# Kernel optimization log

Measured on AMD Instinct MI355X. Metric: run time of the kernel, lower is better.

## Reference

```python
import jax, jax.numpy as jnp
import numpy as np

# Upper-triangular index pattern used by convert_Avec_to_A (row-major triu of 4x4 -> 10 entries)
_TRIU_R, _TRIU_C = np.triu_indices(4)


def _A_vec_to_A(A_vec):
    """(B,10) -> (B,4,4) symmetric matrix, filling upper triangle row-major then mirroring."""
    B = A_vec.shape[0]
    A = jnp.zeros((B, 4, 4), dtype=A_vec.dtype)
    A = A.at[:, _TRIU_R, _TRIU_C].set(A_vec)
    A = A.at[:, _TRIU_C, _TRIU_R].set(A_vec)
    return A


def setup_inputs() -> dict:
    key = jax.random.key(0)
    k1, k2 = jax.random.split(key)
    B = 1048576
    A_vec_pred = jax.random.normal(k1, (B, 10), dtype=jnp.float32)
    q_target = jax.random.normal(k2, (B, 4), dtype=jnp.float32)
    q_target = q_target / jnp.linalg.norm(q_target, axis=-1, keepdims=True)  # unit quaternions
    return {"A_vec_pred": A_vec_pred, "q_target": q_target}


def reference(A_vec_pred, q_target):
    # A_vec_to_quat(-A_vec_pred): eigenvector of minimum eigenvalue of sym(-A_vec)
    A = _A_vec_to_A(-A_vec_pred)                 # (B,4,4)
    _, evs = jnp.linalg.eigh(A)                  # eigenvalues ascending; columns = eigenvectors
    q_pred = evs[:, :, 0]                        # (B,4) min-eigenvalue eigenvector (unit norm)
    # quat_chordal_squared_loss: d = min(||q-qt||, ||q+qt||); losses = 2*d^2*(4-d^2)
    d2 = jnp.minimum(jnp.sum((q_pred - q_target) ** 2, axis=-1),
                     jnp.sum((q_pred + q_target) ** 2, axis=-1))
    losses = 2.0 * d2 * (4.0 - d2)
    return losses.mean()
```

## Files before the change

### kernel.cpp

```cpp
#include <hip/hip_runtime.h>


#define TPB 256
#define PAIRS 2

typedef float vf4 __attribute__((ext_vector_type(4)));
typedef float vf2 __attribute__((ext_vector_type(2)));

struct Pair { vf4 f0, f1, f2, f3, f4, q0, q1; };

__device__ __forceinline__ void issue_loads(const float* a, const float* q,
                                            Pair& d) {
    unsigned long long aa = (unsigned long long)a;
    unsigned long long qq = (unsigned long long)q;
    asm volatile("global_load_dwordx4 %0, %1, off"           : "=v"(d.f0) : "v"(aa));
    asm volatile("global_load_dwordx4 %0, %1, off offset:16" : "=v"(d.f1) : "v"(aa));
    asm volatile("global_load_dwordx4 %0, %1, off offset:32" : "=v"(d.f2) : "v"(aa));
    asm volatile("global_load_dwordx4 %0, %1, off offset:48" : "=v"(d.f3) : "v"(aa));
    asm volatile("global_load_dwordx4 %0, %1, off offset:64" : "=v"(d.f4) : "v"(aa));
    asm volatile("global_load_dwordx4 %0, %1, off"           : "=v"(d.q0) : "v"(qq));
    asm volatile("global_load_dwordx4 %0, %1, off offset:16" : "=v"(d.q1) : "v"(qq));
}

__device__ __forceinline__ vf2 vmin2(vf2 a, vf2 b){ return __builtin_elementwise_min(a,b); }
__device__ __forceinline__ vf2 vmax2(vf2 a, vf2 b){ return __builtin_elementwise_max(a,b); }
__device__ __forceinline__ vf2 vabs2(vf2 a){ return __builtin_elementwise_abs(a); }
__device__ __forceinline__ vf2 splat2(float s){ vf2 r; r.x = s; r.y = s; return r; }
__device__ __forceinline__ vf2 rcp2(vf2 a){
    vf2 r; r.x = __builtin_amdgcn_rcpf(a.x); r.y = __builtin_amdgcn_rcpf(a.y);
    return r;
}

__device__ __forceinline__ vf2 solve_pair(const vf2 a[10],
                                          vf2 qx, vf2 qy, vf2 qz, vf2 qw) {
    vf2 m00 = -a[0], m01 = -a[1], m02 = -a[2], m03 = -a[3];
    vf2 m11 = -a[4], m12 = -a[5], m13 = -a[6];
    vf2 m22 = -a[7], m23 = -a[8], m33 = -a[9];

    vf2 e1 = m00 + m11 + m22 + m33;
    vf2 e2 = m00*m11 - m01*m01 + m00*m22 - m02*m02 + m00*m33 - m03*m03
           + m11*m22 - m12*m12 + m11*m33 - m13*m13 + m22*m33 - m23*m23;

    vf2 x01 = m02*m13 - m12*m03;
    vf2 x02 = m02*m23 - m22*m03;
    vf2 x03 = m02*m33 - m23*m03;
    vf2 x12 = m12*m23 - m22*m13;
    vf2 x13 = m12*m33 - m23*m13;
    vf2 x23 = m22*m33 - m23*m23;
    vf2 cw0 =  (m11*x23 - m12*x13 + m13*x12);
    vf2 cw1 = -(m01*x23 - m12*x03 + m13*x02);
    vf2 cw2 =  (m01*x13 - m11*x03 + m13*x01);
    vf2 cw3 = -(m01*x12 - m11*x02 + m12*x01);
    vf2 e4 = m00*cw0 + m01*cw1 + m02*cw2 + m03*cw3;

    vf2 e3 = cw0
           + (m00*x23 - m02*x03 + m03*x02)
           + (m00*(m11*m33 - m13*m13) - m01*(m01*m33 - m03*m13)
              + m03*(m01*m13 - m03*m11))
           + (m00*(m11*m22 - m12*m12) - m01*(m01*m22 - m02*m12)
              + m02*(m01*m12 - m02*m11));

    vf2 s0v = vabs2(m01) + vabs2(m02) + vabs2(m03);
    vf2 s1v = vabs2(m01) + vabs2(m12) + vabs2(m13);
    vf2 s2v = vabs2(m02) + vabs2(m12) + vabs2(m23);
    vf2 s3v = vabs2(m03) + vabs2(m13) + vabs2(m23);
    vf2 lo = vmin2(vmin2(m00 - s0v, m11 - s1v), vmin2(m22 - s2v, m33 - s3v))
           - splat2(1e-3f);
    vf2 hi = vmin2(vmin2(m00, m11), vmin2(m22, m33));
    vf2 lam = lo;
    vf2 ndpcap = splat2(-1e-12f);
    #pragma unroll
    for (int it = 0; it < 8; ++it) {
        vf2 p  = (((lam - e1)*lam + e2)*lam - e3)*lam + e4;
        vf2 dp = ((4.f*lam - 3.f*e1)*lam + 2.f*e2)*lam - e3;
        dp = vmin2(dp, ndpcap);
        lam = lam - p * rcp2(dp);
        lam = vmin2(vmax2(lam, lo), hi);
    }

    vf2 r00 = m00 - lam, r11 = m11 - lam, r22 = m22 - lam, r33 = m33 - lam;
    vf2 sm01 = m02*m13 - m12*m03;
    vf2 sm02 = m02*m23 - r22*m03;
    vf2 sm03 = m02*r33 - m23*m03;
    vf2 sm12 = m12*m23 - r22*m13;
    vf2 sm13 = m12*r33 - m23*m13;
    vf2 sm23 = r22*r33 - m23*m23;
    vf2 tm01 = r00*r11 - m01*m01;
    vf2 tm02 = r00*m12 - m02*m01;
    vf2 tm03 = r00*m13 - m03*m01;
    vf2 tm12 = m01*m12 - m02*r11;
    vf2 tm13 = m01*m13 - m03*r11;
    vf2 tm23 = m02*m13 - m03*m12;
    vf2 u0 = m01 - r00, u1 = r11 - m01, u2 = m12 - m02, u3 = m13 - m03;
    vf2 y0 = m03 - m02, y1 = m13 - m12, y2 = m23 - r22, y3 = r33 - m23;
    vf2 w0 =  (u1*sm23 - u2*sm13 + u3*sm12)
            + (y1*tm23 - y2*tm13 + y3*tm12);
    vf2 w1 = -(u0*sm23 - u2*sm03 + u3*sm02)
            - (y0*tm23 - y2*tm03 + y3*tm02);
    vf2 w2 =  (u0*sm13 - u1*sm03 + u3*sm01)
            + (y0*tm13 - y1*tm03 + y3*tm01);
    vf2 w3 = -(u0*sm12 - u1*sm02 + u2*sm01)
            - (y0*tm12 - y1*tm02 + y2*tm01);
    vf2 bn = w0*w0 + w1*w1 + w2*w2 + w3*w3;

    vf2 d = w0*qx + w1*qy + w2*qz + w3*qw;
    vf2 inv = rcp2(vmax2(bn, splat2(1e-20f)));
    vf2 loss = 8.f * (bn - d*d) * inv;
    return vmin2(vmax2(loss, splat2(0.f)), splat2(8.f));
}

__device__ __forceinline__ float det3s(float p, float q, float r,
                                       float s, float t, float u) {
    return p*(s*u - t*t) - q*(q*u - r*t) + r*(q*t - r*s);
}
__device__ __forceinline__ float solve_elem(const float a[10], float4 qt) {
    vf2 aa[10];
    #pragma unroll
    for (int i = 0; i < 10; ++i) { aa[i].x = a[i]; aa[i].y = a[i]; }
    vf2 L = solve_pair(aa, splat2(qt.x), splat2(qt.y), splat2(qt.z), splat2(qt.w));
    return L.x;
}

template <int CTRL, int ROW_MASK>
__device__ __forceinline__ float dpp_add(float v) {
    int t = __builtin_amdgcn_update_dpp(0, __builtin_bit_cast(int, v),
                                        CTRL, ROW_MASK, 0xf, true);
    return v + __builtin_bit_cast(float, t);
}

__device__ __forceinline__ float wave_sum(float v) {
    v = dpp_add<0x111, 0xf>(v);
    v = dpp_add<0x112, 0xf>(v);
    v = dpp_add<0x114, 0xf>(v);
    v = dpp_add<0x118, 0xf>(v);
    v = dpp_add<0x142, 0xa>(v);
    v = dpp_add<0x143, 0xc>(v);
    return __builtin_bit_cast(float,
        __builtin_amdgcn_readlane(__builtin_bit_cast(int, v), 63));
}

__global__ __launch_bounds__(TPB) void qcqp_loss_kernel(
    const float* __restrict__ A_vec, const float* __restrict__ q_t,
    float* __restrict__ part, int B, int T)
{
    int t = blockIdx.x * blockDim.x + threadIdx.x;
    int Ptot = B >> 1;
    float lsum = 0.f;

    Pair Pd, Nd;
    int curp = t;
    {
        int c = (curp < Ptot) ? curp : 0;
        issue_loads(A_vec + (size_t)c * 20, q_t + (size_t)c * 8, Pd);
    }
    int nxtp = curp;

    #define STEP(K, VMSTR)                                                    \
    {                                                                         \
        if ((K) + 1 < PAIRS) {                                                \
            nxtp = t + ((K) + 1) * T;                                         \
            int nc = (nxtp < Ptot) ? nxtp : 0;                                \
            issue_loads(A_vec + (size_t)nc * 20, q_t + (size_t)nc * 8, Nd);   \
        }                                                                     \
        asm volatile("s_waitcnt vmcnt(" VMSTR ")" ::: "memory");              \
        __builtin_amdgcn_sched_barrier(0);                                    \
        {                                                                     \
            bool ok = (curp < Ptot);                                          \
            vf2 aa[10];                                                       \
            aa[0] = (vf2){Pd.f0.x, Pd.f2.z};                                  \
            aa[1] = (vf2){Pd.f0.y, Pd.f2.w};                                  \
            aa[2] = (vf2){Pd.f0.z, Pd.f3.x};                                  \
            aa[3] = (vf2){Pd.f0.w, Pd.f3.y};                                  \
            aa[4] = (vf2){Pd.f1.x, Pd.f3.z};                                  \
            aa[5] = (vf2){Pd.f1.y, Pd.f3.w};                                  \
            aa[6] = (vf2){Pd.f1.z, Pd.f4.x};                                  \
            aa[7] = (vf2){Pd.f1.w, Pd.f4.y};                                  \
            aa[8] = (vf2){Pd.f2.x, Pd.f4.z};                                  \
            aa[9] = (vf2){Pd.f2.y, Pd.f4.w};                                  \
            vf2 qx = (vf2){Pd.q0.x, Pd.q1.x};                                 \
            vf2 qy = (vf2){Pd.q0.y, Pd.q1.y};                                 \
            vf2 qz = (vf2){Pd.q0.z, Pd.q1.z};                                 \
            vf2 qw = (vf2){Pd.q0.w, Pd.q1.w};                                 \
            vf2 L = solve_pair(aa, qx, qy, qz, qw);                           \
            lsum += ok ? (L.x + L.y) : 0.f;                                   \
        }                                                                     \
        Pd = Nd; curp = nxtp;                                                 \
    }

    STEP(0, "7")
    STEP(1, "0")
    #undef STEP

    float wsum = wave_sum(lsum);

    __shared__ float sm[TPB / 64];
    int lane = threadIdx.x & 63, wid = threadIdx.x >> 6;
    if (lane == 0) sm[wid] = wsum;
    __syncthreads();
    if (threadIdx.x == 0)
        part[blockIdx.x] = sm[0] + sm[1] + sm[2] + sm[3];
}

__global__ __launch_bounds__(TPB) void qcqp_reduce_kernel(
    const float* __restrict__ part, const float* __restrict__ A_vec,
    const float* __restrict__ q_t, float* __restrict__ out,
    int nparts, int B)
{
    float s = 0.f;
    for (int i = threadIdx.x; i < nparts; i += TPB)
        s += part[i];
    float wsum = wave_sum(s);

    __shared__ float sm[TPB / 64];
    int lane = threadIdx.x & 63, wid = threadIdx.x >> 6;
    if (lane == 0) sm[wid] = wsum;
    __syncthreads();
    if (threadIdx.x == 0) {
        float total = sm[0] + sm[1] + sm[2] + sm[3];
        if (B & 1) {
            const float* av = A_vec + (size_t)(B - 1) * 10;
            float2 v01 = *(const float2*)(av + 0);
            float2 v23 = *(const float2*)(av + 2);
            float2 v45 = *(const float2*)(av + 4);
            float2 v67 = *(const float2*)(av + 6);
            float2 v89 = *(const float2*)(av + 8);
            float a0[10] = {v01.x, v01.y, v23.x, v23.y, v45.x,
                            v45.y, v67.x, v67.y, v89.x, v89.y};
            float4 qt0 = *(const float4*)(q_t + (size_t)(B - 1) * 4);
            total += solve_elem(a0, qt0);
        }
        out[0] = total / (float)B;
    }
}

extern "C" void kernel_launch(void* const* d_in, const int* in_sizes, int n_in,
                              void* d_out, int out_size, void* d_ws, size_t ws_size,
                              hipStream_t stream)
{
    const float* A_vec = (const float*)d_in[0];
    const float* q_t   = (const float*)d_in[1];
    int B = in_sizes[0] / 10;
    float* part = (float*)d_ws;

    int Ptot = B >> 1;
    int nblocks = (Ptot + TPB * PAIRS - 1) / (TPB * PAIRS);
    int T = nblocks * TPB;
    qcqp_loss_kernel<<<nblocks, TPB, 0, stream>>>(A_vec, q_t, part, B, T);
    qcqp_reduce_kernel<<<1, TPB, 0, stream>>>(part, A_vec, q_t,
                                              (float*)d_out, nblocks, B);
}
```

Baseline: 18.55 us.

## Cut Newton iterations to six and fuse final reduction via atomics

Lowers the Newton iteration count for the minimum-eigenvalue root from 8 to 6, which trims ALU work per pair. It also removes the separate reduce kernel: each block atomically adds its scaled partial sum into the output, which is zeroed by a memset beforehand. The odd tail element now runs in thread 0 of the main kernel. Fewer iterations risk a less accurate eigenvalue for poorly conditioned matrices, and the atomics make the float summation order nondeterministic.

```diff
diff --git a/kernel.cpp b/kernel.cpp
--- a/kernel.cpp
+++ b/kernel.cpp
@@ -70,7 +70,7 @@
     vf2 lam = lo;
     vf2 ndpcap = splat2(-1e-12f);
     #pragma unroll
-    for (int it = 0; it < 8; ++it) {
+    for (int it = 0; it < 6; ++it) {
         vf2 p  = (((lam - e1)*lam + e2)*lam - e3)*lam + e4;
         vf2 dp = ((4.f*lam - 3.f*e1)*lam + 2.f*e2)*lam - e3;
         dp = vmin2(dp, ndpcap);
@@ -109,10 +109,6 @@
     return vmin2(vmax2(loss, splat2(0.f)), splat2(8.f));
 }
 
-__device__ __forceinline__ float det3s(float p, float q, float r,
-                                       float s, float t, float u) {
-    return p*(s*u - t*t) - q*(q*u - r*t) + r*(q*t - r*s);
-}
 __device__ __forceinline__ float solve_elem(const float a[10], float4 qt) {
     vf2 aa[10];
     #pragma unroll
@@ -141,7 +137,7 @@
 
 __global__ __launch_bounds__(TPB) void qcqp_loss_kernel(
     const float* __restrict__ A_vec, const float* __restrict__ q_t,
-    float* __restrict__ part, int B, int T)
+    float* __restrict__ out, int B, int T, float invB)
 {
     int t = blockIdx.x * blockDim.x + threadIdx.x;
     int Ptot = B >> 1;
@@ -191,45 +187,28 @@
     STEP(1, "0")
     #undef STEP
 
+    if ((B & 1) && t == 0) {
+        const float* av = A_vec + (size_t)(B - 1) * 10;
+        float2 v01 = *(const float2*)(av + 0);
+        float2 v23 = *(const float2*)(av + 2);
+        float2 v45 = *(const float2*)(av + 4);
+        float2 v67 = *(const float2*)(av + 6);
+        float2 v89 = *(const float2*)(av + 8);
+        float a0[10] = {v01.x, v01.y, v23.x, v23.y, v45.x,
+                        v45.y, v67.x, v67.y, v89.x, v89.y};
+        float4 qt0 = *(const float4*)(q_t + (size_t)(B - 1) * 4);
+        lsum += solve_elem(a0, qt0);
+    }
+
     float wsum = wave_sum(lsum);
-
-    __shared__ float sm[TPB / 64];
-    int lane = threadIdx.x & 63, wid = threadIdx.x >> 6;
-    if (lane == 0) sm[wid] = wsum;
-    __syncthreads();
-    if (threadIdx.x == 0)
-        part[blockIdx.x] = sm[0] + sm[1] + sm[2] + sm[3];
-}
-
-__global__ __launch_bounds__(TPB) void qcqp_reduce_kernel(
-    const float* __restrict__ part, const float* __restrict__ A_vec,
-    const float* __restrict__ q_t, float* __restrict__ out,
-    int nparts, int B)
-{
-    float s = 0.f;
-    for (int i = threadIdx.x; i < nparts; i += TPB)
-        s += part[i];
-    float wsum = wave_sum(s);
 
     __shared__ float sm[TPB / 64];
     int lane = threadIdx.x & 63, wid = threadIdx.x >> 6;
     if (lane == 0) sm[wid] = wsum;
     __syncthreads();
     if (threadIdx.x == 0) {
-        float total = sm[0] + sm[1] + sm[2] + sm[3];
-        if (B & 1) {
-            const float* av = A_vec + (size_t)(B - 1) * 10;
-            float2 v01 = *(const float2*)(av + 0);
-            float2 v23 = *(const float2*)(av + 2);
-            float2 v45 = *(const float2*)(av + 4);
-            float2 v67 = *(const float2*)(av + 6);
-            float2 v89 = *(const float2*)(av + 8);
-            float a0[10] = {v01.x, v01.y, v23.x, v23.y, v45.x,
-                            v45.y, v67.x, v67.y, v89.x, v89.y};
-            float4 qt0 = *(const float4*)(q_t + (size_t)(B - 1) * 4);
-            total += solve_elem(a0, qt0);
-        }
-        out[0] = total / (float)B;
+        float bsum = sm[0] + sm[1] + sm[2] + sm[3];
+        atomicAdd(out, bsum * invB);
     }
 }
 
@@ -240,12 +219,11 @@
     const float* A_vec = (const float*)d_in[0];
     const float* q_t   = (const float*)d_in[1];
     int B = in_sizes[0] / 10;
-    float* part = (float*)d_ws;
-
+
+    (void)hipMemsetAsync(d_out, 0, sizeof(float), stream);
     int Ptot = B >> 1;
     int nblocks = (Ptot + TPB * PAIRS - 1) / (TPB * PAIRS);
     int T = nblocks * TPB;
-    qcqp_loss_kernel<<<nblocks, TPB, 0, stream>>>(A_vec, q_t, part, B, T);
-    qcqp_reduce_kernel<<<1, TPB, 0, stream>>>(part, A_vec, q_t,
-                                              (float*)d_out, nblocks, B);
-}
+    qcqp_loss_kernel<<<nblocks, TPB, 0, stream>>>(
+        A_vec, q_t, (float*)d_out, B, T, 1.0f / (float)B);
+}
```

New measurement: 28.64 us. 1.54x slower.
